# Optimization experiments

Hardware: AMD Instinct MI355X
Metric: run time of the kernel (lower is better)

## Reference

```python
import jax, jax.numpy as jnp
import numpy as np

N_HEAD = 16

def setup_inputs() -> dict:
    key = jax.random.key(0)
    ks = jax.random.split(key, 5)
    B, T, C = 2, 2048, 1024
    s = 1.0 / np.sqrt(C)
    return {
        "x": jax.random.normal(ks[0], (B, T, C), dtype=jnp.float32),
        "Wq": jax.random.normal(ks[1], (C, C), dtype=jnp.float32) * s,
        "Wk": jax.random.normal(ks[2], (C, C), dtype=jnp.float32) * s,
        "Wv": jax.random.normal(ks[3], (C, C), dtype=jnp.float32) * s,
        "Wo": jax.random.normal(ks[4], (C, C), dtype=jnp.float32) * s,
        "bo": jnp.zeros((C,), dtype=jnp.float32),
    }

def reference(x, Wq, Wk, Wv, Wo, bo):
    B, T, C = x.shape
    H = N_HEAD
    D = C // H

    def shape(t):  # (B,T,C) -> (B,H,T,D)
        return t.reshape(B, T, H, D).transpose(0, 2, 1, 3)

    q = shape(x @ Wq)
    k = shape(x @ Wk)
    v = shape(x @ Wv)

    # scores: (B,H,T,Tk), Tk == T (no past_kv)
    att = jnp.einsum("bhtd,bhsd->bhts", q, k) * (1.0 / np.sqrt(D))
    i = jnp.arange(T)[:, None]
    j = jnp.arange(T)[None, :]
    causal = (j <= i)  # (T, Tk)
    att = jnp.where(causal[None, None], att, -jnp.inf)
    att = jax.nn.softmax(att, axis=-1)  # dropout=0.0 -> identity

    out = jnp.einsum("bhts,bhsd->bhtd", att, v)
    out = out.transpose(0, 2, 1, 3).reshape(B, T, C)
    out = out @ Wo + bo
    return out, (k, v)
```

## Files before the change

kernel.cpp:

```cpp
#include <hip/hip_runtime.h>
#include <hip/hip_bf16.h>

constexpr int B_ = 2;
constexpr int T_ = 2048;
constexpr int C_ = 1024;
constexpr int H_ = 16;
constexpr int D_ = 64;
constexpr int M_ = B_ * T_;

typedef __attribute__((ext_vector_type(8))) short bf16x8;
typedef __attribute__((ext_vector_type(4))) float f32x4;
typedef const __attribute__((address_space(1))) void gaddr_t;
typedef __attribute__((address_space(3))) void laddr_t;

__device__ __forceinline__ unsigned short f2bf(float f) {
    unsigned u = __float_as_uint(f);
    return (unsigned short)((u + 0x7fffu + ((u >> 16) & 1u)) >> 16);
}

union BF8 { bf16x8 v; __hip_bfloat162 h[4]; };

__device__ __forceinline__ bf16x8 cvt8(const float4 a, const float4 b) {
    BF8 r;
    r.h[0] = __float22bfloat162_rn(make_float2(a.x, a.y));
    r.h[1] = __float22bfloat162_rn(make_float2(a.z, a.w));
    r.h[2] = __float22bfloat162_rn(make_float2(b.x, b.y));
    r.h[3] = __float22bfloat162_rn(make_float2(b.z, b.w));
    return r.v;
}

__global__ __launch_bounds__(256)
void cast_x(const float* __restrict__ x, unsigned short* __restrict__ xb, int n4)
{
    for (int i = blockIdx.x * 256 + threadIdx.x; i < n4; i += gridDim.x * 256) {
        float4 v = ((const float4*)x)[i];
        union { __hip_bfloat162 h[2]; ushort4 u; } o;
        o.h[0] = __float22bfloat162_rn(make_float2(v.x, v.y));
        o.h[1] = __float22bfloat162_rn(make_float2(v.z, v.w));
        ((ushort4*)xb)[i] = o.u;
    }
}

__global__ __launch_bounds__(256)
void tcast_w(const float* __restrict__ Wq, const float* __restrict__ Wk,
             const float* __restrict__ Wv, const float* __restrict__ Wo,
             unsigned short* __restrict__ wtb)
{
    __shared__ float tile[64][65];
    const int z = blockIdx.z;
    const float* W = (z == 0) ? Wq : (z == 1) ? Wk : (z == 2) ? Wv : Wo;
    unsigned short* O = wtb + (size_t)z * C_ * C_;

    const int tid = threadIdx.x;
    const int n0 = blockIdx.x * 64, k0 = blockIdx.y * 64;
    const int r = tid >> 4, c4 = (tid & 15) * 4;

#pragma unroll
    for (int i = 0; i < 4; ++i) {
        const int kk = i * 16 + r;
        float4 v = *(const float4*)(W + (size_t)(k0 + kk) * C_ + n0 + c4);
        tile[c4 + 0][kk] = v.x;
        tile[c4 + 1][kk] = v.y;
        tile[c4 + 2][kk] = v.z;
        tile[c4 + 3][kk] = v.w;
    }
    __syncthreads();
#pragma unroll
    for (int i = 0; i < 4; ++i) {
        const int nn = i * 16 + r;
        ushort4 o;
        o.x = f2bf(tile[nn][c4 + 0]);
        o.y = f2bf(tile[nn][c4 + 1]);
        o.z = f2bf(tile[nn][c4 + 2]);
        o.w = f2bf(tile[nn][c4 + 3]);
        *(ushort4*)(O + (size_t)(n0 + nn) * C_ + k0 + c4) = o;
    }
}

template<int WRITE_KB>
__global__ __launch_bounds__(256)
void gemm_qkv(const unsigned short* __restrict__ xb, const unsigned short* __restrict__ wtb,
              unsigned short* __restrict__ qb, float* __restrict__ kout,
              float* __restrict__ vout, unsigned short* __restrict__ kb,
              unsigned short* __restrict__ vtt)
{
    __shared__ unsigned short As[128 * 64];
    __shared__ unsigned short Bs[128 * 64];

    const int tid = threadIdx.x;
    const int which = blockIdx.x >> 3;
    const int n0 = (blockIdx.x & 7) * 128;
    const int m0 = blockIdx.y * 128;
    const unsigned short* wt = wtb + (size_t)which * C_ * C_;

    const int lane = tid & 63, w = tid >> 6;
    const int wm = (w >> 1) * 64, wn = (w & 1) * 64;
    const int fr = lane & 15, qd = lane >> 4;

    f32x4 acc[4][4] = {};

    for (int k0 = 0; k0 < C_; k0 += 64) {
#pragma unroll
        for (int cc = 0; cc < 4; ++cc) {
            const int c = tid + cc * 256;
            const int row = c >> 3, dg = (c & 7) ^ (row & 7);
            __builtin_amdgcn_global_load_lds(
                (gaddr_t*)(xb + (size_t)(m0 + row) * C_ + k0 + dg * 8),
                (laddr_t*)((char*)As + (size_t)c * 16), 16, 0, 0);
        }
#pragma unroll
        for (int cc = 0; cc < 4; ++cc) {
            const int c = tid + cc * 256;
            const int row = c >> 3, dg = (c & 7) ^ (row & 7);
            __builtin_amdgcn_global_load_lds(
                (gaddr_t*)(wt + (size_t)(n0 + row) * C_ + k0 + dg * 8),
                (laddr_t*)((char*)Bs + (size_t)c * 16), 16, 0, 0);
        }
        __syncthreads();

#pragma unroll
        for (int half = 0; half < 2; ++half) {
            bf16x8 af[4], bfv[4];
#pragma unroll
            for (int mt = 0; mt < 4; ++mt) {
                const int row = wm + mt * 16 + fr, dg = half * 4 + qd;
                af[mt] = *(const bf16x8*)&As[row * 64 + ((dg ^ (row & 7)) * 8)];
            }
#pragma unroll
            for (int nt = 0; nt < 4; ++nt) {
                const int row = wn + nt * 16 + fr, dg = half * 4 + qd;
                bfv[nt] = *(const bf16x8*)&Bs[row * 64 + ((dg ^ (row & 7)) * 8)];
            }
#pragma unroll
            for (int mt = 0; mt < 4; ++mt)
#pragma unroll
                for (int nt = 0; nt < 4; ++nt)
                    acc[mt][nt] = __builtin_amdgcn_mfma_f32_16x16x32_bf16(
                        bfv[nt], af[mt], acc[mt][nt], 0, 0, 0);
        }
        __syncthreads();
    }

#pragma unroll
    for (int mt = 0; mt < 4; ++mt) {
        const int mm = m0 + wm + mt * 16 + fr;
        const int b = mm >> 11, t = mm & (T_ - 1);
#pragma unroll
        for (int nt = 0; nt < 4; ++nt) {
            const int nn = n0 + wn + nt * 16 + qd * 4;
            const int h = nn >> 6, d0 = nn & 63;
            const int bh = b * H_ + h;
            const size_t off = ((size_t)bh * T_ + t) * D_ + d0;
            const f32x4 a4 = acc[mt][nt];
            if (which == 0) {
                *(ushort4*)(qb + off) =
                    make_ushort4(f2bf(a4[0]), f2bf(a4[1]), f2bf(a4[2]), f2bf(a4[3]));
            } else if (which == 1) {
                *(float4*)(kout + off) = make_float4(a4[0], a4[1], a4[2], a4[3]);
                if (WRITE_KB)
                    *(ushort4*)(kb + off) =
                        make_ushort4(f2bf(a4[0]), f2bf(a4[1]), f2bf(a4[2]), f2bf(a4[3]));
            } else {
                *(float4*)(vout + off) = make_float4(a4[0], a4[1], a4[2], a4[3]);
                unsigned short* vb = vtt
                    + (((size_t)bh * (T_ / 64) + (t >> 6)) * 64 + d0) * 64 + (t & 63);
#pragma unroll
                for (int r = 0; r < 4; ++r) vb[(size_t)r * 64] = f2bf(a4[r]);
            }
        }
    }
}

__global__ __launch_bounds__(256)
void gemm_o(const unsigned short* __restrict__ ab, const unsigned short* __restrict__ wot,
            const float* __restrict__ bo, float* __restrict__ out)
{
    __shared__ unsigned short As[128 * 64];
    __shared__ unsigned short Bs[128 * 64];

    const int tid = threadIdx.x;
    const int n0 = blockIdx.x * 128;
    const int m0 = blockIdx.y * 128;

    const int lane = tid & 63, w = tid >> 6;
    const int wm = (w >> 1) * 64, wn = (w & 1) * 64;
    const int fr = lane & 15, qd = lane >> 4;

    f32x4 acc[4][4] = {};

    for (int k0 = 0; k0 < C_; k0 += 64) {
#pragma unroll
        for (int cc = 0; cc < 4; ++cc) {
            const int c = tid + cc * 256;
            const int row = c >> 3, dg = (c & 7) ^ (row & 7);
            __builtin_amdgcn_global_load_lds(
                (gaddr_t*)(ab + (size_t)(m0 + row) * C_ + k0 + dg * 8),
                (laddr_t*)((char*)As + (size_t)c * 16), 16, 0, 0);
        }
#pragma unroll
        for (int cc = 0; cc < 4; ++cc) {
            const int c = tid + cc * 256;
            const int row = c >> 3, dg = (c & 7) ^ (row & 7);
            __builtin_amdgcn_global_load_lds(
                (gaddr_t*)(wot + (size_t)(n0 + row) * C_ + k0 + dg * 8),
                (laddr_t*)((char*)Bs + (size_t)c * 16), 16, 0, 0);
        }
        __syncthreads();

#pragma unroll
        for (int half = 0; half < 2; ++half) {
            bf16x8 af[4], bfv[4];
#pragma unroll
            for (int mt = 0; mt < 4; ++mt) {
                const int row = wm + mt * 16 + fr, dg = half * 4 + qd;
                af[mt] = *(const bf16x8*)&As[row * 64 + ((dg ^ (row & 7)) * 8)];
            }
#pragma unroll
            for (int nt = 0; nt < 4; ++nt) {
                const int row = wn + nt * 16 + fr, dg = half * 4 + qd;
                bfv[nt] = *(const bf16x8*)&Bs[row * 64 + ((dg ^ (row & 7)) * 8)];
            }
#pragma unroll
            for (int mt = 0; mt < 4; ++mt)
#pragma unroll
                for (int nt = 0; nt < 4; ++nt)
                    acc[mt][nt] = __builtin_amdgcn_mfma_f32_16x16x32_bf16(
                        bfv[nt], af[mt], acc[mt][nt], 0, 0, 0);
        }
        __syncthreads();
    }

#pragma unroll
    for (int mt = 0; mt < 4; ++mt) {
        const int mm = m0 + wm + mt * 16 + fr;
#pragma unroll
        for (int nt = 0; nt < 4; ++nt) {
            const int nn = n0 + wn + nt * 16 + qd * 4;
            const float4 b4 = *(const float4*)(bo + nn);
            *(float4*)(out + (size_t)mm * C_ + nn) =
                make_float4(acc[mt][nt][0] + b4.x, acc[mt][nt][1] + b4.y,
                            acc[mt][nt][2] + b4.z, acc[mt][nt][3] + b4.w);
        }
    }
}

__global__ __launch_bounds__(256)
void attn_lds(const unsigned short* __restrict__ qb, const unsigned short* __restrict__ kb,
              const unsigned short* __restrict__ vtt, unsigned short* __restrict__ attb)
{
    __shared__ unsigned short Ks[2][64 * 64];
    __shared__ unsigned short Vs[2][64 * 64];
    __shared__ alignas(16) unsigned short Pt[4][16 * 72];

    const int tid = threadIdx.x;
    const int lane = tid & 63, w = tid >> 6;
    const int fr = lane & 15, qd = lane >> 4;

    const int blk = blockIdx.x;
    const int xcd = blk & 7, within = blk >> 3;
    const int bh = xcd * 4 + (within & 3);
    const int jj = within >> 2;
    const int kk_ = jj >> 3, ii_ = jj & 7;
    const int qt = (kk_ == 0) ? (31 - ii_) : (kk_ == 1) ? ii_
                 : (kk_ == 2) ? (23 - ii_) : (8 + ii_);
    const int b = bh >> 4, h = bh & 15;

    unsigned short* Pw = Pt[w];
    const unsigned short* qB = qb  + (size_t)bh * T_ * D_;
    const unsigned short* kB = kb  + (size_t)bh * T_ * D_;
    const unsigned short* vT = vtt + (size_t)bh * (T_ / 64) * 64 * 64;

    const int qr0 = qt * 64 + w * 16;
    const int qrow_g = qr0 + fr;

    bf16x8 aq0 = *(const bf16x8*)(qB + (size_t)(qr0 + fr) * D_ + qd * 8);
    bf16x8 aq1 = *(const bf16x8*)(qB + (size_t)(qr0 + fr) * D_ + 32 + qd * 8);

    f32x4 accT[4] = {};
    float l_i = 0.0f;
    const float sc2 = 0.18033688f;

    const int L0 = w * 128 + lane, L1 = L0 + 64;
    const int r0 = L0 >> 3, e0 = (((L0 & 7) ^ (r0 & 7)) * 8);
    const int r1 = L1 >> 3, e1 = (((L1 & 7) ^ (r1 & 7)) * 8);

    {
        __builtin_amdgcn_global_load_lds((gaddr_t*)(kB + r0 * 64 + e0),
            (laddr_t*)((char*)Ks[0] + (size_t)L0 * 16), 16, 0, 0);
        __builtin_amdgcn_global_load_lds((gaddr_t*)(kB + r1 * 64 + e1),
            (laddr_t*)((char*)Ks[0] + (size_t)L1 * 16), 16, 0, 0);
        __builtin_amdgcn_global_load_lds((gaddr_t*)(vT + r0 * 64 + e0),
            (laddr_t*)((char*)Vs[0] + (size_t)L0 * 16), 16, 0, 0);
        __builtin_amdgcn_global_load_lds((gaddr_t*)(vT + r1 * 64 + e1),
            (laddr_t*)((char*)Vs[0] + (size_t)L1 * 16), 16, 0, 0);
    }
    asm volatile("s_waitcnt vmcnt(0)" ::: "memory");
    __builtin_amdgcn_s_barrier();
    __builtin_amdgcn_sched_barrier(0);

    for (int jt = 0; jt <= qt; ++jt) {
        const int cur = jt & 1;
        if (jt < qt) {
            const unsigned short* kt = kB + (size_t)((jt + 1) * 64) * 64;
            const unsigned short* vt = vT + (size_t)(jt + 1) * 4096;
            char* Kn = (char*)Ks[cur ^ 1];
            char* Vn = (char*)Vs[cur ^ 1];
            __builtin_amdgcn_global_load_lds((gaddr_t*)(kt + r0 * 64 + e0),
                (laddr_t*)(Kn + (size_t)L0 * 16), 16, 0, 0);
            __builtin_amdgcn_global_load_lds((gaddr_t*)(kt + r1 * 64 + e1),
                (laddr_t*)(Kn + (size_t)L1 * 16), 16, 0, 0);
            __builtin_amdgcn_global_load_lds((gaddr_t*)(vt + r0 * 64 + e0),
                (laddr_t*)(Vn + (size_t)L0 * 16), 16, 0, 0);
            __builtin_amdgcn_global_load_lds((gaddr_t*)(vt + r1 * 64 + e1),
                (laddr_t*)(Vn + (size_t)L1 * 16), 16, 0, 0);
        }
        const unsigned short* Kc = Ks[cur];
        const unsigned short* Vc = Vs[cur];

        bf16x8 bk[8];
#pragma unroll
        for (int q8 = 0; q8 < 8; ++q8) {
            const int row = (q8 >> 1) * 16 + fr;
            const int dg = (q8 & 1) * 4 + qd;
            bk[q8] = *(const bf16x8*)&Kc[row * 64 + ((dg ^ (row & 7)) * 8)];
        }

        f32x4 s4[4] = {};
        __builtin_amdgcn_s_setprio(1);
#pragma unroll
        for (int nt = 0; nt < 4; ++nt) {
            s4[nt] = __builtin_amdgcn_mfma_f32_16x16x32_bf16(bk[nt * 2 + 0], aq0, s4[nt], 0, 0, 0);
            s4[nt] = __builtin_amdgcn_mfma_f32_16x16x32_bf16(bk[nt * 2 + 1], aq1, s4[nt], 0, 0, 0);
        }
        __builtin_amdgcn_s_setprio(0);

        if (jt == qt) {
            const int kbase = jt * 64 + qd * 4;
#pragma unroll
            for (int nt = 0; nt < 4; ++nt)
#pragma unroll
            for (int r = 0; r < 4; ++r) {
                const int kcol = kbase + nt * 16 + r;
                const float pv = (kcol <= qrow_g)
                               ? __builtin_amdgcn_exp2f(s4[nt][r] * sc2) : 0.0f;
                s4[nt][r] = pv;
                l_i += pv;
            }
        } else {
#pragma unroll
            for (int nt = 0; nt < 4; ++nt)
#pragma unroll
            for (int r = 0; r < 4; ++r) {
                const float pv = __builtin_amdgcn_exp2f(s4[nt][r] * sc2);
                s4[nt][r] = pv;
                l_i += pv;
            }
        }

#pragma unroll
        for (int nt = 0; nt < 4; ++nt) {
            union { __hip_bfloat162 h2[2]; unsigned long long u; } pk;
            pk.h2[0] = __float22bfloat162_rn(make_float2(s4[nt][0], s4[nt][1]));
            pk.h2[1] = __float22bfloat162_rn(make_float2(s4[nt][2], s4[nt][3]));
            *(unsigned long long*)&Pw[fr * 72 + nt * 16 + qd * 4] = pk.u;
        }
        const bf16x8 ap0 = *(const bf16x8*)&Pw[fr * 72 + qd * 8];
        const bf16x8 ap1 = *(const bf16x8*)&Pw[fr * 72 + 32 + qd * 8];

        bf16x8 bv[8];
#pragma unroll
        for (int q8 = 0; q8 < 8; ++q8) {
            const int row = (q8 >> 1) * 16 + fr;
            const int dg = (q8 & 1) * 4 + qd;
            bv[q8] = *(const bf16x8*)&Vc[row * 64 + ((dg ^ (row & 7)) * 8)];
        }

        __builtin_amdgcn_s_setprio(1);
#pragma unroll
        for (int nt = 0; nt < 4; ++nt) {
            accT[nt] = __builtin_amdgcn_mfma_f32_16x16x32_bf16(bv[nt * 2 + 0], ap0, accT[nt], 0, 0, 0);
            accT[nt] = __builtin_amdgcn_mfma_f32_16x16x32_bf16(bv[nt * 2 + 1], ap1, accT[nt], 0, 0, 0);
        }
        __builtin_amdgcn_s_setprio(0);

        asm volatile("s_waitcnt vmcnt(0)" ::: "memory");
        __builtin_amdgcn_s_barrier();
        __builtin_amdgcn_sched_barrier(0);
    }

    l_i += __shfl_xor(l_i, 16);
    l_i += __shfl_xor(l_i, 32);
    const float inv = 1.0f / l_i;

#pragma unroll
    for (int nt = 0; nt < 4; ++nt) {
        union { __hip_bfloat162 h2[2]; unsigned long long u; } ok;
        ok.h2[0] = __float22bfloat162_rn(make_float2(accT[nt][0] * inv, accT[nt][1] * inv));
        ok.h2[1] = __float22bfloat162_rn(make_float2(accT[nt][2] * inv, accT[nt][3] * inv));
        *(unsigned long long*)&Pw[fr * 72 + nt * 16 + qd * 4] = ok.u;
    }
    {
        const int row = lane >> 2, d0 = (lane & 3) * 16;
        const bf16x8 o0 = *(const bf16x8*)&Pw[row * 72 + d0];
        const bf16x8 o1 = *(const bf16x8*)&Pw[row * 72 + d0 + 8];
        unsigned short* op = attb + ((size_t)b * T_ + qr0 + row) * C_ + h * 64 + d0;
        *(bf16x8*)op = o0;
        *(bf16x8*)(op + 8) = o1;
    }
}

__global__ __launch_bounds__(256)
void attn_v4(const unsigned short* __restrict__ qb, const float* __restrict__ kf,
             const unsigned short* __restrict__ vtt, unsigned short* __restrict__ attb)
{
    __shared__ alignas(16) unsigned short Pt[4][16 * 72];

    const int tid = threadIdx.x;
    const int lane = tid & 63, w = tid >> 6;
    const int fr = lane & 15, qd = lane >> 4;

    const int blk = blockIdx.x;
    const int xcd = blk & 7, within = blk >> 3;
    const int bh = xcd * 4 + (within & 3);
    const int jj = within >> 2;
    const int kk_ = jj >> 3, ii_ = jj & 7;
    const int qt = (kk_ == 0) ? (31 - ii_) : (kk_ == 1) ? ii_
                 : (kk_ == 2) ? (23 - ii_) : (8 + ii_);
    const int b = bh >> 4, h = bh & 15;

    unsigned short* Pw = Pt[w];
    const unsigned short* qB = qb  + (size_t)bh * T_ * D_;
    const float*          kB = kf  + (size_t)bh * T_ * D_;
    const unsigned short* vT = vtt + (size_t)bh * (T_ / 64) * 64 * 64;

    const int qr0 = qt * 64 + w * 16;
    const int qrow_g = qr0 + fr;

    bf16x8 aq0 = *(const bf16x8*)(qB + (size_t)(qr0 + fr) * D_ + qd * 8);
    bf16x8 aq1 = *(const bf16x8*)(qB + (size_t)(qr0 + fr) * D_ + 32 + qd * 8);

    f32x4 accT[4] = {};
    float l_i = 0.0f;
    const float sc2 = 0.18033688f;

    for (int jt = 0; jt <= qt; ++jt) {
        bf16x8 bk[8];
#pragma unroll
        for (int q8 = 0; q8 < 8; ++q8) {
            const float* p = kB + (size_t)(jt * 64 + (q8 >> 1) * 16 + fr) * D_
                           + (q8 & 1) * 32 + qd * 8;
            bk[q8] = cvt8(*(const float4*)p, *(const float4*)(p + 4));
        }
        f32x4 s4[4] = {};
#pragma unroll
        for (int nt = 0; nt < 4; ++nt) {
            s4[nt] = __builtin_amdgcn_mfma_f32_16x16x32_bf16(bk[nt * 2 + 0], aq0, s4[nt], 0, 0, 0);
            s4[nt] = __builtin_amdgcn_mfma_f32_16x16x32_bf16(bk[nt * 2 + 1], aq1, s4[nt], 0, 0, 0);
        }
        if (jt == qt) {
            const int kbase = jt * 64 + qd * 4;
#pragma unroll
            for (int nt = 0; nt < 4; ++nt)
#pragma unroll
            for (int r = 0; r < 4; ++r) {
                const int kcol = kbase + nt * 16 + r;
                const float pv = (kcol <= qrow_g)
                               ? __builtin_amdgcn_exp2f(s4[nt][r] * sc2) : 0.0f;
                s4[nt][r] = pv; l_i += pv;
            }
        } else {
#pragma unroll
            for (int nt = 0; nt < 4; ++nt)
#pragma unroll
            for (int r = 0; r < 4; ++r) {
                const float pv = __builtin_amdgcn_exp2f(s4[nt][r] * sc2);
                s4[nt][r] = pv; l_i += pv;
            }
        }
#pragma unroll
        for (int nt = 0; nt < 4; ++nt) {
            union { __hip_bfloat162 h2[2]; unsigned long long u; } pk;
            pk.h2[0] = __float22bfloat162_rn(make_float2(s4[nt][0], s4[nt][1]));
            pk.h2[1] = __float22bfloat162_rn(make_float2(s4[nt][2], s4[nt][3]));
            *(unsigned long long*)&Pw[fr * 72 + nt * 16 + qd * 4] = pk.u;
        }
        const bf16x8 ap0 = *(const bf16x8*)&Pw[fr * 72 + qd * 8];
        const bf16x8 ap1 = *(const bf16x8*)&Pw[fr * 72 + 32 + qd * 8];

        bf16x8 bv[8];
#pragma unroll
        for (int q8 = 0; q8 < 8; ++q8)
            bv[q8] = *(const bf16x8*)(vT + (size_t)jt * 4096
                                      + ((q8 >> 1) * 16 + fr) * 64 + (q8 & 1) * 32 + qd * 8);
#pragma unroll
        for (int nt = 0; nt < 4; ++nt) {
            accT[nt] = __builtin_amdgcn_mfma_f32_16x16x32_bf16(bv[nt * 2 + 0], ap0, accT[nt], 0, 0, 0);
            accT[nt] = __builtin_amdgcn_mfma_f32_16x16x32_bf16(bv[nt * 2 + 1], ap1, accT[nt], 0, 0, 0);
        }
    }

    l_i += __shfl_xor(l_i, 16);
    l_i += __shfl_xor(l_i, 32);
    const float inv = 1.0f / l_i;
#pragma unroll
    for (int nt = 0; nt < 4; ++nt) {
        union { __hip_bfloat162 h2[2]; unsigned long long u; } ok;
        ok.h2[0] = __float22bfloat162_rn(make_float2(accT[nt][0] * inv, accT[nt][1] * inv));
        ok.h2[1] = __float22bfloat162_rn(make_float2(accT[nt][2] * inv, accT[nt][3] * inv));
        *(unsigned long long*)&Pw[fr * 72 + nt * 16 + qd * 4] = ok.u;
    }
    {
        const int row = lane >> 2, d0 = (lane & 3) * 16;
        const bf16x8 o0 = *(const bf16x8*)&Pw[row * 72 + d0];
        const bf16x8 o1 = *(const bf16x8*)&Pw[row * 72 + d0 + 8];
        unsigned short* op = attb + ((size_t)b * T_ + qr0 + row) * C_ + h * 64 + d0;
        *(bf16x8*)op = o0;
        *(bf16x8*)(op + 8) = o1;
    }
}

extern "C" void kernel_launch(void* const* d_in, const int* in_sizes, int n_in,
                              void* d_out, int out_size, void* d_ws, size_t ws_size,
                              hipStream_t stream)
{
    (void)in_sizes; (void)n_in; (void)out_size;
    const float* x  = (const float*)d_in[0];
    const float* Wq = (const float*)d_in[1];
    const float* Wk = (const float*)d_in[2];
    const float* Wv = (const float*)d_in[3];
    const float* Wo = (const float*)d_in[4];
    const float* bo = (const float*)d_in[5];

    float* out  = (float*)d_out;
    float* kout = out  + (size_t)M_ * C_;
    float* vout = kout + (size_t)B_ * H_ * T_ * D_;

    unsigned short* xb   = (unsigned short*)d_ws;
    unsigned short* wtb  = xb  + (size_t)M_ * C_;
    unsigned short* qb   = wtb + (size_t)4 * C_ * C_;
    unsigned short* vtt  = qb  + (size_t)M_ * C_;
    unsigned short* kb   = vtt + (size_t)M_ * C_;
    unsigned short* attb = xb;
    const bool use_kb = ws_size >= (size_t)40 * 1024 * 1024;

    cast_x<<<1024, 256, 0, stream>>>(x, xb, (M_ * C_) / 4);
    tcast_w<<<dim3(16, 16, 4), 256, 0, stream>>>(Wq, Wk, Wv, Wo, wtb);

    if (use_kb)
        gemm_qkv<1><<<dim3(24, M_ / 128), 256, 0, stream>>>(xb, wtb, qb, kout, vout, kb, vtt);
    else
        gemm_qkv<0><<<dim3(24, M_ / 128), 256, 0, stream>>>(xb, wtb, qb, kout, vout, kb, vtt);

    if (use_kb)
        attn_lds<<<1024, 256, 0, stream>>>(qb, kb, vtt, attb);
    else
        attn_v4<<<1024, 256, 0, stream>>>(qb, kout, vtt, attb);

    gemm_o<<<dim3(8, M_ / 128), 256, 0, stream>>>(attb, wtb + (size_t)3 * C_ * C_, bo, out);
}
```

Baseline: 202.7 us.

## Double-buffer LDS tiles in QKV and output projection GEMMs

Both projection GEMMs now keep two LDS buffers for A and B. Each iteration issues the next k-tile's global_load_lds into the spare buffer before computing on the current one, using explicit vmcnt waits and raw barriers in place of __syncthreads. This is meant to hide global load latency behind the MFMA work. In exchange LDS use doubles to 64KB per block, which may reduce occupancy, and correctness now depends on the hand-written waitcnt counts.

New measurement: 199.7 us. Within noise of the previous version (-1.5%).

```diff
diff --git a/kernel.cpp b/kernel.cpp
--- a/kernel.cpp
+++ b/kernel.cpp
@@ -84,8 +84,8 @@
               float* __restrict__ vout, unsigned short* __restrict__ kb,
               unsigned short* __restrict__ vtt)
 {
-    __shared__ unsigned short As[128 * 64];
-    __shared__ unsigned short Bs[128 * 64];
+    __shared__ unsigned short As[2][128 * 64];
+    __shared__ unsigned short Bs[2][128 * 64];
 
     const int tid = threadIdx.x;
     const int which = blockIdx.x >> 3;
@@ -97,39 +97,57 @@
     const int wm = (w >> 1) * 64, wn = (w & 1) * 64;
     const int fr = lane & 15, qd = lane >> 4;
 
+    int crow[4], cofs[4]; size_t clds[4];
+#pragma unroll
+    for (int cc = 0; cc < 4; ++cc) {
+        const int c = tid + cc * 256;
+        crow[cc] = c >> 3;
+        cofs[cc] = ((c & 7) ^ (crow[cc] & 7)) * 8;
+        clds[cc] = (size_t)c * 16;
+    }
+
+#define STAGE_QKV(pb, k0v)                                                        \
+    {                                                                             \
+        _Pragma("unroll")                                                         \
+        for (int cc = 0; cc < 4; ++cc)                                            \
+            __builtin_amdgcn_global_load_lds(                                     \
+                (gaddr_t*)(xb + (size_t)(m0 + crow[cc]) * C_ + (k0v) + cofs[cc]), \
+                (laddr_t*)((char*)As[pb] + clds[cc]), 16, 0, 0);                  \
+        _Pragma("unroll")                                                         \
+        for (int cc = 0; cc < 4; ++cc)                                            \
+            __builtin_amdgcn_global_load_lds(                                     \
+                (gaddr_t*)(wt + (size_t)(n0 + crow[cc]) * C_ + (k0v) + cofs[cc]), \
+                (laddr_t*)((char*)Bs[pb] + clds[cc]), 16, 0, 0);                  \
+    }
+
     f32x4 acc[4][4] = {};
 
-    for (int k0 = 0; k0 < C_; k0 += 64) {
-#pragma unroll
-        for (int cc = 0; cc < 4; ++cc) {
-            const int c = tid + cc * 256;
-            const int row = c >> 3, dg = (c & 7) ^ (row & 7);
-            __builtin_amdgcn_global_load_lds(
-                (gaddr_t*)(xb + (size_t)(m0 + row) * C_ + k0 + dg * 8),
-                (laddr_t*)((char*)As + (size_t)c * 16), 16, 0, 0);
-        }
-#pragma unroll
-        for (int cc = 0; cc < 4; ++cc) {
-            const int c = tid + cc * 256;
-            const int row = c >> 3, dg = (c & 7) ^ (row & 7);
-            __builtin_amdgcn_global_load_lds(
-                (gaddr_t*)(wt + (size_t)(n0 + row) * C_ + k0 + dg * 8),
-                (laddr_t*)((char*)Bs + (size_t)c * 16), 16, 0, 0);
-        }
-        __syncthreads();
-
+    STAGE_QKV(0, 0);
+    for (int kt = 0; kt < C_ / 64; ++kt) {
+        const int pb = kt & 1;
+        if (kt + 1 < C_ / 64) {
+            STAGE_QKV(pb ^ 1, (kt + 1) * 64);
+            asm volatile("s_waitcnt vmcnt(8)" ::: "memory");
+        } else {
+            asm volatile("s_waitcnt vmcnt(0)" ::: "memory");
+        }
+        __builtin_amdgcn_s_barrier();
+        __builtin_amdgcn_sched_barrier(0);
+
+        const unsigned short* Ac = As[pb];
+        const unsigned short* Bc = Bs[pb];
 #pragma unroll
         for (int half = 0; half < 2; ++half) {
             bf16x8 af[4], bfv[4];
 #pragma unroll
             for (int mt = 0; mt < 4; ++mt) {
                 const int row = wm + mt * 16 + fr, dg = half * 4 + qd;
-                af[mt] = *(const bf16x8*)&As[row * 64 + ((dg ^ (row & 7)) * 8)];
+                af[mt] = *(const bf16x8*)&Ac[row * 64 + ((dg ^ (row & 7)) * 8)];
             }
 #pragma unroll
             for (int nt = 0; nt < 4; ++nt) {
                 const int row = wn + nt * 16 + fr, dg = half * 4 + qd;
-                bfv[nt] = *(const bf16x8*)&Bs[row * 64 + ((dg ^ (row & 7)) * 8)];
+                bfv[nt] = *(const bf16x8*)&Bc[row * 64 + ((dg ^ (row & 7)) * 8)];
             }
 #pragma unroll
             for (int mt = 0; mt < 4; ++mt)
@@ -138,8 +156,10 @@
                     acc[mt][nt] = __builtin_amdgcn_mfma_f32_16x16x32_bf16(
                         bfv[nt], af[mt], acc[mt][nt], 0, 0, 0);
         }
-        __syncthreads();
-    }
+        __builtin_amdgcn_sched_barrier(0);
+        __builtin_amdgcn_s_barrier();
+    }
+#undef STAGE_QKV
 
 #pragma unroll
     for (int mt = 0; mt < 4; ++mt) {
@@ -175,8 +195,8 @@
 void gemm_o(const unsigned short* __restrict__ ab, const unsigned short* __restrict__ wot,
             const float* __restrict__ bo, float* __restrict__ out)
 {
-    __shared__ unsigned short As[128 * 64];
-    __shared__ unsigned short Bs[128 * 64];
+    __shared__ unsigned short As[2][128 * 64];
+    __shared__ unsigned short Bs[2][128 * 64];
 
     const int tid = threadIdx.x;
     const int n0 = blockIdx.x * 128;
@@ -186,39 +206,57 @@
     const int wm = (w >> 1) * 64, wn = (w & 1) * 64;
     const int fr = lane & 15, qd = lane >> 4;
 
+    int crow[4], cofs[4]; size_t clds[4];
+#pragma unroll
+    for (int cc = 0; cc < 4; ++cc) {
+        const int c = tid + cc * 256;
+        crow[cc] = c >> 3;
+        cofs[cc] = ((c & 7) ^ (crow[cc] & 7)) * 8;
+        clds[cc] = (size_t)c * 16;
+    }
+
+#define STAGE_O(pb, k0v)                                                          \
+    {                                                                             \
+        _Pragma("unroll")                                                         \
+        for (int cc = 0; cc < 4; ++cc)                                            \
+            __builtin_amdgcn_global_load_lds(                                     \
+                (gaddr_t*)(ab + (size_t)(m0 + crow[cc]) * C_ + (k0v) + cofs[cc]), \
+                (laddr_t*)((char*)As[pb] + clds[cc]), 16, 0, 0);                  \
+        _Pragma("unroll")                                                         \
+        for (int cc = 0; cc < 4; ++cc)                                            \
+            __builtin_amdgcn_global_load_lds(                                     \
+                (gaddr_t*)(wot + (size_t)(n0 + crow[cc]) * C_ + (k0v) + cofs[cc]),\
+                (laddr_t*)((char*)Bs[pb] + clds[cc]), 16, 0, 0);                  \
+    }
+
     f32x4 acc[4][4] = {};
 
-    for (int k0 = 0; k0 < C_; k0 += 64) {
-#pragma unroll
-        for (int cc = 0; cc < 4; ++cc) {
-            const int c = tid + cc * 256;
-            const int row = c >> 3, dg = (c & 7) ^ (row & 7);
-            __builtin_amdgcn_global_load_lds(
-                (gaddr_t*)(ab + (size_t)(m0 + row) * C_ + k0 + dg * 8),
-                (laddr_t*)((char*)As + (size_t)c * 16), 16, 0, 0);
-        }
-#pragma unroll
-        for (int cc = 0; cc < 4; ++cc) {
-            const int c = tid + cc * 256;
-            const int row = c >> 3, dg = (c & 7) ^ (row & 7);
-            __builtin_amdgcn_global_load_lds(
-                (gaddr_t*)(wot + (size_t)(n0 + row) * C_ + k0 + dg * 8),
-                (laddr_t*)((char*)Bs + (size_t)c * 16), 16, 0, 0);
-        }
-        __syncthreads();
-
+    STAGE_O(0, 0);
+    for (int kt = 0; kt < C_ / 64; ++kt) {
+        const int pb = kt & 1;
+        if (kt + 1 < C_ / 64) {
+            STAGE_O(pb ^ 1, (kt + 1) * 64);
+            asm volatile("s_waitcnt vmcnt(8)" ::: "memory");
+        } else {
+            asm volatile("s_waitcnt vmcnt(0)" ::: "memory");
+        }
+        __builtin_amdgcn_s_barrier();
+        __builtin_amdgcn_sched_barrier(0);
+
+        const unsigned short* Ac = As[pb];
+        const unsigned short* Bc = Bs[pb];
 #pragma unroll
         for (int half = 0; half < 2; ++half) {
             bf16x8 af[4], bfv[4];
 #pragma unroll
             for (int mt = 0; mt < 4; ++mt) {
                 const int row = wm + mt * 16 + fr, dg = half * 4 + qd;
-                af[mt] = *(const bf16x8*)&As[row * 64 + ((dg ^ (row & 7)) * 8)];
+                af[mt] = *(const bf16x8*)&Ac[row * 64 + ((dg ^ (row & 7)) * 8)];
             }
 #pragma unroll
             for (int nt = 0; nt < 4; ++nt) {
                 const int row = wn + nt * 16 + fr, dg = half * 4 + qd;
-                bfv[nt] = *(const bf16x8*)&Bs[row * 64 + ((dg ^ (row & 7)) * 8)];
+                bfv[nt] = *(const bf16x8*)&Bc[row * 64 + ((dg ^ (row & 7)) * 8)];
             }
 #pragma unroll
             for (int mt = 0; mt < 4; ++mt)
@@ -227,8 +265,10 @@
                     acc[mt][nt] = __builtin_amdgcn_mfma_f32_16x16x32_bf16(
                         bfv[nt], af[mt], acc[mt][nt], 0, 0, 0);
         }
-        __syncthreads();
-    }
+        __builtin_amdgcn_sched_barrier(0);
+        __builtin_amdgcn_s_barrier();
+    }
+#undef STAGE_O
 
 #pragma unroll
     for (int mt = 0; mt < 4; ++mt) {
```

## Fuse prep casts, remap GEMM blocks across XCDs, shrink output GEMM N-tile

Applied to the files above, without the earlier changes.

Merges the x cast and the weight transpose-cast into one launch: z-slice 4 casts x and slices 0-3 transpose the weights. Remaps block indices in the QKV and output GEMMs so consecutive hardware blocks, which are spread across the 8 XCDs, get contiguous tiles, aiming for better L2 reuse. Halves the output GEMM N-tile to 64 so it launches 512 blocks instead of 256, filling more CUs at the cost of reloading each A tile twice as often.

Result: faster. 191.6 us (-5.5%).

```diff
diff --git a/kernel.cpp b/kernel.cpp
--- a/kernel.cpp
+++ b/kernel.cpp
@@ -30,28 +30,32 @@
 }
 
 __global__ __launch_bounds__(256)
-void cast_x(const float* __restrict__ x, unsigned short* __restrict__ xb, int n4)
+void prep(const float* __restrict__ x, const float* __restrict__ Wq,
+          const float* __restrict__ Wk, const float* __restrict__ Wv,
+          const float* __restrict__ Wo, unsigned short* __restrict__ xb,
+          unsigned short* __restrict__ wtb)
 {
-    for (int i = blockIdx.x * 256 + threadIdx.x; i < n4; i += gridDim.x * 256) {
-        float4 v = ((const float4*)x)[i];
-        union { __hip_bfloat162 h[2]; ushort4 u; } o;
-        o.h[0] = __float22bfloat162_rn(make_float2(v.x, v.y));
-        o.h[1] = __float22bfloat162_rn(make_float2(v.z, v.w));
-        ((ushort4*)xb)[i] = o.u;
-    }
-}
-
-__global__ __launch_bounds__(256)
-void tcast_w(const float* __restrict__ Wq, const float* __restrict__ Wk,
-             const float* __restrict__ Wv, const float* __restrict__ Wo,
-             unsigned short* __restrict__ wtb)
-{
+    const int z = blockIdx.z;
+    const int tid = threadIdx.x;
+
+    if (z == 4) {
+        const int base = (blockIdx.y * 16 + blockIdx.x) * 4096 + tid;
+#pragma unroll
+        for (int i = 0; i < 16; ++i) {
+            const int idx = base + i * 256;
+            float4 v = ((const float4*)x)[idx];
+            union { __hip_bfloat162 h[2]; ushort4 u; } o;
+            o.h[0] = __float22bfloat162_rn(make_float2(v.x, v.y));
+            o.h[1] = __float22bfloat162_rn(make_float2(v.z, v.w));
+            ((ushort4*)xb)[idx] = o.u;
+        }
+        return;
+    }
+
     __shared__ float tile[64][65];
-    const int z = blockIdx.z;
     const float* W = (z == 0) ? Wq : (z == 1) ? Wk : (z == 2) ? Wv : Wo;
     unsigned short* O = wtb + (size_t)z * C_ * C_;
 
-    const int tid = threadIdx.x;
     const int n0 = blockIdx.x * 64, k0 = blockIdx.y * 64;
     const int r = tid >> 4, c4 = (tid & 15) * 4;
 
@@ -88,9 +92,13 @@
     __shared__ unsigned short Bs[128 * 64];
 
     const int tid = threadIdx.x;
-    const int which = blockIdx.x >> 3;
-    const int n0 = (blockIdx.x & 7) * 128;
-    const int m0 = blockIdx.y * 128;
+
+    const int flat = blockIdx.y * 24 + blockIdx.x;
+    const int l = (flat & 7) * 96 + (flat >> 3);
+    const int m0 = (l / 24) * 128;
+    const int xc = l % 24;
+    const int which = xc >> 3;
+    const int n0 = (xc & 7) * 128;
     const unsigned short* wt = wtb + (size_t)which * C_ * C_;
 
     const int lane = tid & 63, w = tid >> 6;
@@ -176,17 +184,20 @@
             const float* __restrict__ bo, float* __restrict__ out)
 {
     __shared__ unsigned short As[128 * 64];
-    __shared__ unsigned short Bs[128 * 64];
+    __shared__ unsigned short Bs[64 * 64];
 
     const int tid = threadIdx.x;
-    const int n0 = blockIdx.x * 128;
-    const int m0 = blockIdx.y * 128;
+
+    const int flat = blockIdx.y * 16 + blockIdx.x;
+    const int l = (flat & 7) * 64 + (flat >> 3);
+    const int m0 = (l / 16) * 128;
+    const int n0 = (l % 16) * 64;
 
     const int lane = tid & 63, w = tid >> 6;
-    const int wm = (w >> 1) * 64, wn = (w & 1) * 64;
+    const int wm = (w >> 1) * 64, wn = (w & 1) * 32;
     const int fr = lane & 15, qd = lane >> 4;
 
-    f32x4 acc[4][4] = {};
+    f32x4 acc[4][2] = {};
 
     for (int k0 = 0; k0 < C_; k0 += 64) {
 #pragma unroll
@@ -198,7 +209,7 @@
                 (laddr_t*)((char*)As + (size_t)c * 16), 16, 0, 0);
         }
 #pragma unroll
-        for (int cc = 0; cc < 4; ++cc) {
+        for (int cc = 0; cc < 2; ++cc) {
             const int c = tid + cc * 256;
             const int row = c >> 3, dg = (c & 7) ^ (row & 7);
             __builtin_amdgcn_global_load_lds(
@@ -209,21 +220,21 @@
 
 #pragma unroll
         for (int half = 0; half < 2; ++half) {
-            bf16x8 af[4], bfv[4];
+            bf16x8 af[4], bfv[2];
 #pragma unroll
             for (int mt = 0; mt < 4; ++mt) {
                 const int row = wm + mt * 16 + fr, dg = half * 4 + qd;
                 af[mt] = *(const bf16x8*)&As[row * 64 + ((dg ^ (row & 7)) * 8)];
             }
 #pragma unroll
-            for (int nt = 0; nt < 4; ++nt) {
+            for (int nt = 0; nt < 2; ++nt) {
                 const int row = wn + nt * 16 + fr, dg = half * 4 + qd;
                 bfv[nt] = *(const bf16x8*)&Bs[row * 64 + ((dg ^ (row & 7)) * 8)];
             }
 #pragma unroll
             for (int mt = 0; mt < 4; ++mt)
 #pragma unroll
-                for (int nt = 0; nt < 4; ++nt)
+                for (int nt = 0; nt < 2; ++nt)
                     acc[mt][nt] = __builtin_amdgcn_mfma_f32_16x16x32_bf16(
                         bfv[nt], af[mt], acc[mt][nt], 0, 0, 0);
         }
@@ -234,7 +245,7 @@
     for (int mt = 0; mt < 4; ++mt) {
         const int mm = m0 + wm + mt * 16 + fr;
 #pragma unroll
-        for (int nt = 0; nt < 4; ++nt) {
+        for (int nt = 0; nt < 2; ++nt) {
             const int nn = n0 + wn + nt * 16 + qd * 4;
             const float4 b4 = *(const float4*)(bo + nn);
             *(float4*)(out + (size_t)mm * C_ + nn) =
@@ -543,18 +554,17 @@
     unsigned short* attb = xb;
     const bool use_kb = ws_size >= (size_t)40 * 1024 * 1024;
 
-    cast_x<<<1024, 256, 0, stream>>>(x, xb, (M_ * C_) / 4);
-    tcast_w<<<dim3(16, 16, 4), 256, 0, stream>>>(Wq, Wk, Wv, Wo, wtb);
+    prep<<<dim3(16, 16, 5), 256, 0, stream>>>(x, Wq, Wk, Wv, Wo, xb, wtb);
 
     if (use_kb)
-        gemm_qkv<1><<<dim3(24, M_ / 128), 256, 0, stream>>>(xb, wtb, qb, kout, vout, kb, vtt);
+        gemm_qkv<1><<<dim3(24, 32), 256, 0, stream>>>(xb, wtb, qb, kout, vout, kb, vtt);
     else
-        gemm_qkv<0><<<dim3(24, M_ / 128), 256, 0, stream>>>(xb, wtb, qb, kout, vout, kb, vtt);
+        gemm_qkv<0><<<dim3(24, 32), 256, 0, stream>>>(xb, wtb, qb, kout, vout, kb, vtt);
 
     if (use_kb)
         attn_lds<<<1024, 256, 0, stream>>>(qb, kb, vtt, attb);
     else
         attn_v4<<<1024, 256, 0, stream>>>(qb, kout, vtt, attb);
 
-    gemm_o<<<dim3(8, M_ / 128), 256, 0, stream>>>(attb, wtb + (size_t)3 * C_ * C_, bo, out);
-}
+    gemm_o<<<dim3(16, 32), 256, 0, stream>>>(attb, wtb + (size_t)3 * C_ * C_, bo, out);
+}
```
